# Performance work log

Hardware: AMD Instinct MI355X
Metric: run time of the kernel (lower is better)

## Reference

```python
import jax, jax.numpy as jnp
import numpy as np

INPUT_SIZE = (224, 224)


def setup_inputs() -> dict:
    key = jax.random.key(0)
    k1, k2, k3 = jax.random.split(key, 3)
    feat2 = jax.random.normal(k1, (16, 512, 28, 28), dtype=jnp.float32)
    feat3 = jax.random.normal(k2, (16, 1024, 14, 14), dtype=jnp.float32)
    memory_bank = jax.random.normal(k3, (16384, 1536), dtype=jnp.float32)
    return {"feat2": feat2, "feat3": feat3, "memory_bank": memory_bank}


def reference(feat2, feat3, memory_bank):
    b, c2, h, w = feat2.shape
    c3 = feat3.shape[1]
    # interpolate(feat3, size=(h,w), mode='bilinear', align_corners=False)
    feat3_up = jax.image.resize(feat3, (b, c3, h, w), method='bilinear')
    features = jnp.concatenate([feat2, feat3_up], axis=1)  # [b, c, h, w]
    c = c2 + c3
    feats = features.transpose(0, 2, 3, 1).reshape(-1, c)  # [N, c]
    x_sq = jnp.sum(feats * feats, axis=1, keepdims=True)            # [N, 1]
    m_sq = jnp.sum(memory_bank * memory_bank, axis=1)[None, :]      # [1, M]
    d2 = x_sq + m_sq - 2.0 * (feats @ memory_bank.T)                # [N, M]
    min_d = jnp.sqrt(jnp.maximum(jnp.min(d2, axis=1), 0.0))         # [N]
    anomaly_map = min_d.reshape(b, 1, h, w)
    anomaly_map = jax.image.resize(
        anomaly_map, (b, 1, INPUT_SIZE[0], INPUT_SIZE[1]), method='bilinear')
    pred_score = jnp.max(anomaly_map.reshape(b, -1), axis=1)
    return anomaly_map, pred_score
```

## Files before the change

kernel.cpp:

```cpp
#include <hip/hip_runtime.h>
#include <math.h>

#define N_ROWS 12544
#define C_DIM  1536
#define M_ROWS 16384
#define BATCH  16

#define QS    16.0f
#define S2x2  0.0078125f
#define S2    0.00390625f

typedef int   i32x4 __attribute__((ext_vector_type(4)));
typedef unsigned char u8;
typedef signed char   i8;

__device__ __forceinline__ unsigned fkey(float f) {
  unsigned u = __float_as_uint(f);
  return (u & 0x80000000u) ? ~u : (u | 0x80000000u);
}
__device__ __forceinline__ float funkey(unsigned k) {
  unsigned u = (k & 0x80000000u) ? (k ^ 0x80000000u) : ~k;
  return __uint_as_float(u);
}

__device__ __forceinline__ void gl_lds16(const void* g, void* l) {
  __builtin_amdgcn_global_load_lds(
      (__attribute__((address_space(1))) void*)(g),
      (__attribute__((address_space(3))) void*)(l), 16, 0, 0);
}

__device__ __forceinline__ int quant(float v) {
  int q = __float2int_rn(v * QS);
  return max(-127, min(127, q));
}

#define FSTRIDE 528

__global__ __launch_bounds__(512) void prep_all(
    const float* __restrict__ feat2, const float* __restrict__ feat3,
    const float* __restrict__ mb,
    i8* __restrict__ feats, i8* __restrict__ mbb,
    int* __restrict__ xsqp, float* __restrict__ msq,
    unsigned* __restrict__ dmin, unsigned* __restrict__ score) {
  const int blk = blockIdx.x;
  const int t = threadIdx.x;
  __shared__ u8 fsm[28 * FSTRIDE];
  __shared__ int sxq[28];

  if (blk >= 1344) {
    const int wave = t >> 6, lane = t & 63;
    const int row = (blk - 1344) * 8 + wave;
    const float* in = mb + (size_t)row * C_DIM;
    i8* outp = mbb + (size_t)row * C_DIM;
    float ssq = 0.f;
#pragma unroll
    for (int i = 0; i < 6; i++) {
      const int f4 = lane + 64 * i;
      const float4 v = *(const float4*)(in + f4 * 4);
      int q0 = quant(v.x), q1 = quant(v.y), q2 = quant(v.z), q3 = quant(v.w);
      unsigned w = (unsigned)(q0 & 0xFF) | ((unsigned)(q1 & 0xFF) << 8)
                 | ((unsigned)(q2 & 0xFF) << 16) | ((unsigned)(q3 & 0xFF) << 24);
      *(unsigned*)(outp + f4 * 4) = w;
      ssq += (float)(q0*q0 + q1*q1 + q2*q2 + q3*q3);
    }
    for (int off = 32; off > 0; off >>= 1) ssq += __shfl_down(ssq, off, 64);
    if (lane == 0) msq[row] = S2 * ssq;
  } else {
    const int half = blk % 3, p = blk / 3;
    const int b = p / 28, y = p % 28;
    const int n0 = b * 784 + y * 28;

    const float sy = 0.5f * y - 0.25f;
    const int y0 = (int)floorf(sy); const float fy = sy - (float)y0;
    const int y0c = max(y0, 0), y1c = min(y0 + 1, 13);
    const float wy0 = 1.f - fy, wy1 = fy;

    const int g  = t >> 5;
    const int l2 = t & 31;
    const float sx = 0.5f * l2 - 0.25f;
    const int x0 = (int)floorf(sx); const float fx = sx - (float)x0;
    const int x0c = max(x0, 0), x1c = min(x0 + 1, 13);
    const float wx0 = 1.f - fx, wx1 = fx;

    if (t < 28) sxq[t] = 0;

    if (half == 0) {
      const float* f2b = feat2 + (size_t)b * 512 * 784 + y * 28;
#pragma unroll 4
      for (int i = 0; i < 32; i++) {
        const int c = i * 16 + g;
        if (l2 < 28) {
          float v = f2b[(size_t)c * 784 + l2];
          fsm[l2 * FSTRIDE + c] = (u8)(i8)quant(v);
        }
      }
    } else {
      const int cc0 = (half - 1) * 512;
      const float* f3b = feat3 + (size_t)b * 1024 * 196;
#pragma unroll 4
      for (int i = 0; i < 32; i++) {
        const int cc = cc0 + i * 16 + g;
        const float* f3 = f3b + (size_t)cc * 196;
        float v = 0.f;
        if (l2 < 14)       v = f3[y0c * 14 + l2];
        else if (l2 < 28)  v = f3[y1c * 14 + (l2 - 14)];
        float t0 = wy0 * __shfl(v, x0c, 32)     + wy1 * __shfl(v, 14 + x0c, 32);
        float t1 = wy0 * __shfl(v, x1c, 32)     + wy1 * __shfl(v, 14 + x1c, 32);
        if (l2 < 28) {
          float o = wx0 * t0 + wx1 * t1;
          fsm[l2 * FSTRIDE + (i * 16 + g)] = (u8)(i8)quant(o);
        }
      }
    }
    __syncthreads();

    const int c0 = half * 512;
    i8* orow = feats + (size_t)n0 * C_DIM + c0;
    for (int idx = t; idx < 28 * 32; idx += 512) {
      const int row = idx / 32, col = idx % 32;
      i32x4 wv = *(const i32x4*)(fsm + row * FSTRIDE + col * 16);
      *(i32x4*)(orow + (size_t)row * C_DIM + col * 16) = wv;
      int s = 0;
#pragma unroll
      for (int k = 0; k < 4; k++) {
        const int w = wv[k];
        const int b0 = (int)(i8)(w & 0xFF), b1 = (int)(i8)((w >> 8) & 0xFF);
        const int b2 = (int)(i8)((w >> 16) & 0xFF), b3 = (int)(i8)(w >> 24);
        s += b0*b0 + b1*b1 + b2*b2 + b3*b3;
      }
      atomicAdd(&sxq[row], s);
    }
    __syncthreads();
    if (t < 28) {
      xsqp[half * N_ROWS + n0 + t] = sxq[t];
      if (half == 0) dmin[n0 + t] = 0xFFFFFFFFu;
    }
    if (blk == 0 && t < BATCH) score[t] = 0u;
  }
}

__global__ void gemm_min(const i8* __restrict__ X, const i8* __restrict__ Mb,
                         const float* __restrict__ msq,
                         unsigned* __restrict__ dmin) {
  __shared__ u8 As[16384];
  __shared__ u8 Bs[16384];
  __shared__ unsigned smin[128];
  const int t = threadIdx.x;
  const int bx = blockIdx.x;
  const int mtile = ((bx & 7) << 4) | (bx >> 3);
  const int ntile = blockIdx.y;
  const int lane = t & 63, wave = t >> 6;
  const int wm = wave >> 1, wn = wave & 1;
  if (t < 128) smin[t] = 0xFFFFFFFFu;

  const int row0 = ntile * 128;
  const int col0 = mtile * 128;
  const int s_row = t >> 2;
  const int s_ch  = (t & 3) ^ ((t >> 3) & 3);
  const i8* ga = X  + (size_t)(row0 + s_row) * C_DIM + s_ch * 16;
  const i8* gb = Mb + (size_t)(col0 + s_row) * C_DIM + s_ch * 16;
  u8* la = As + t * 16;
  u8* lb = Bs + t * 16;

  i32x4 acc[4][4];
  const i32x4 zero = {0, 0, 0, 0};
#pragma unroll
  for (int mi = 0; mi < 4; mi++)
#pragma unroll
    for (int ni = 0; ni < 4; ni++) acc[mi][ni] = zero;

  const int quad = lane >> 4, l16 = lane & 15;
  const int fsw = (l16 >> 1) & 3;
  const int slot = ((quad ^ fsw) * 16);
  const u8* arow = As + (wm * 64 + l16) * 64 + slot;
  const u8* brow = Bs + (wn * 64 + l16) * 64 + slot;

  for (int k0 = 0; k0 < C_DIM; k0 += 128) {
    __syncthreads();
    gl_lds16(ga + k0,                    la);
    gl_lds16(ga + 64 * C_DIM + k0,       la + 4096);
    gl_lds16(ga + k0 + 64,               la + 8192);
    gl_lds16(ga + 64 * C_DIM + k0 + 64,  la + 12288);
    gl_lds16(gb + k0,                    lb);
    gl_lds16(gb + 64 * C_DIM + k0,       lb + 4096);
    gl_lds16(gb + k0 + 64,               lb + 8192);
    gl_lds16(gb + 64 * C_DIM + k0 + 64,  lb + 12288);
    __syncthreads();
#pragma unroll
    for (int sub = 0; sub < 2; sub++) {
      i32x4 af[4], bf[4];
#pragma unroll
      for (int mi = 0; mi < 4; mi++)
        af[mi] = *(const i32x4*)(arow + sub * 8192 + mi * 1024);
#pragma unroll
      for (int ni = 0; ni < 4; ni++)
        bf[ni] = *(const i32x4*)(brow + sub * 8192 + ni * 1024);
#pragma unroll
      for (int mi = 0; mi < 4; mi++)
#pragma unroll
        for (int ni = 0; ni < 4; ni++)
          acc[mi][ni] = __builtin_amdgcn_mfma_i32_16x16x64_i8(
              af[mi], bf[ni], acc[mi][ni], 0, 0, 0);
    }
  }

  float msql[4];
#pragma unroll
  for (int ni = 0; ni < 4; ni++)
    msql[ni] = msq[col0 + wn * 64 + ni * 16 + l16];

#pragma unroll
  for (int mi = 0; mi < 4; mi++) {
#pragma unroll
    for (int r = 0; r < 4; r++) {
      float v = msql[0] - S2x2 * (float)acc[mi][0][r];
#pragma unroll
      for (int ni = 1; ni < 4; ni++)
        v = fminf(v, msql[ni] - S2x2 * (float)acc[mi][ni][r]);
      v = fminf(v, __shfl_xor(v, 1, 64));
      v = fminf(v, __shfl_xor(v, 2, 64));
      v = fminf(v, __shfl_xor(v, 4, 64));
      v = fminf(v, __shfl_xor(v, 8, 64));
      if (l16 == 0) {
        int lrow = wm * 64 + mi * 16 + quad * 4 + r;
        atomicMin(&smin[lrow], fkey(v));
      }
    }
  }
  __syncthreads();
  if (t < 128) atomicMin(&dmin[row0 + t], smin[t]);
}

__global__ void finalize(const unsigned* __restrict__ dmin,
                         const int* __restrict__ xsqp,
                         float* __restrict__ out) {
  const int b = blockIdx.x, slice = blockIdx.y, t = threadIdx.x;
  __shared__ float smap[784];
  __shared__ float sred[4];
  for (int i = t; i < 784; i += 256) {
    const int idx = b * 784 + i;
    const int xs = xsqp[idx] + xsqp[N_ROWS + idx] + xsqp[2 * N_ROWS + idx];
    float d2 = S2 * (float)xs + funkey(dmin[idx]);
    smap[i] = sqrtf(fmaxf(d2, 0.f));
  }
  __syncthreads();
  float* omap = out + (size_t)b * 50176;
  float tmax = 0.f;
  const int p0 = slice * 6272;
  for (int p = p0 + t; p < p0 + 6272; p += 256) {
    const int Y = p / 224, Xp = p % 224;
    const float sy = Y * 0.125f - 0.4375f;
    const float sx = Xp * 0.125f - 0.4375f;
    const int y0 = (int)floorf(sy); const float fy = sy - (float)y0;
    const int x0 = (int)floorf(sx); const float fx = sx - (float)x0;
    const int y0c = max(y0, 0), y1c = min(y0 + 1, 27);
    const int x0c = max(x0, 0), x1c = min(x0 + 1, 27);
    float v = (1.f-fy)*((1.f-fx)*smap[y0c*28+x0c] + fx*smap[y0c*28+x1c])
            +      fy *((1.f-fx)*smap[y1c*28+x0c] + fx*smap[y1c*28+x1c]);
    omap[p] = v;
    tmax = fmaxf(tmax, v);
  }
  for (int off = 32; off > 0; off >>= 1)
    tmax = fmaxf(tmax, __shfl_down(tmax, off, 64));
  if ((t & 63) == 0) sred[t >> 6] = tmax;
  __syncthreads();
  if (t == 0) {
    float m = fmaxf(fmaxf(sred[0], sred[1]), fmaxf(sred[2], sred[3]));
    atomicMax((unsigned*)(out + 802816 + b), __float_as_uint(m));
  }
}

extern "C" void kernel_launch(void* const* d_in, const int* in_sizes, int n_in,
                              void* d_out, int out_size, void* d_ws, size_t ws_size,
                              hipStream_t stream) {
  const float* feat2 = (const float*)d_in[0];
  const float* feat3 = (const float*)d_in[1];
  const float* mb    = (const float*)d_in[2];
  char* ws = (char*)d_ws;
  i8*       feats = (i8*)ws;
  i8*       mbb   = (i8*)(ws + 19267584);
  int*      xsqp  = (int*)(ws + 44433408);
  float*    msq   = (float*)(ws + 44583936);
  unsigned* dmin  = (unsigned*)(ws + 44649472);
  float* out = (float*)d_out;

  prep_all<<<1344 + 2048, 512, 0, stream>>>(
      feat2, feat3, mb, feats, mbb, xsqp, msq, dmin,
      (unsigned*)(out + 802816));
  gemm_min<<<dim3(128, 98), 256, 0, stream>>>(feats, mbb, msq, dmin);
  finalize<<<dim3(BATCH, 8), 256, 0, stream>>>(dmin, xsqp, out);
}
```

Measured before the change: 507.4 us.

## Double-buffer GEMM LDS tiles with async prefetch and manual vmcnt waits

Restructures the int8 GEMM main loop into a two-buffer software pipeline over 64-wide K slices. The next slice is loaded global-to-LDS while the current slice runs on MFMA, with explicit s_waitcnt vmcnt and s_barrier in place of paired __syncthreads. The aim is to hide global load latency behind matrix compute. It also adds launch_bounds(256). The risk is correctness of the hand-placed waits and barriers, plus extra barrier count per K step.

```diff
diff --git a/kernel.cpp b/kernel.cpp
--- a/kernel.cpp
+++ b/kernel.cpp
@@ -139,9 +139,9 @@
   }
 }
 
-__global__ void gemm_min(const i8* __restrict__ X, const i8* __restrict__ Mb,
-                         const float* __restrict__ msq,
-                         unsigned* __restrict__ dmin) {
+__global__ __launch_bounds__(256) void gemm_min(
+    const i8* __restrict__ X, const i8* __restrict__ Mb,
+    const float* __restrict__ msq, unsigned* __restrict__ dmin) {
   __shared__ u8 As[16384];
   __shared__ u8 Bs[16384];
   __shared__ unsigned smin[128];
@@ -175,34 +175,52 @@
   const u8* arow = As + (wm * 64 + l16) * 64 + slot;
   const u8* brow = Bs + (wn * 64 + l16) * 64 + slot;
 
-  for (int k0 = 0; k0 < C_DIM; k0 += 128) {
-    __syncthreads();
-    gl_lds16(ga + k0,                    la);
-    gl_lds16(ga + 64 * C_DIM + k0,       la + 4096);
-    gl_lds16(ga + k0 + 64,               la + 8192);
-    gl_lds16(ga + 64 * C_DIM + k0 + 64,  la + 12288);
-    gl_lds16(gb + k0,                    lb);
-    gl_lds16(gb + 64 * C_DIM + k0,       lb + 4096);
-    gl_lds16(gb + k0 + 64,               lb + 8192);
-    gl_lds16(gb + 64 * C_DIM + k0 + 64,  lb + 12288);
-    __syncthreads();
-#pragma unroll
-    for (int sub = 0; sub < 2; sub++) {
-      i32x4 af[4], bf[4];
-#pragma unroll
-      for (int mi = 0; mi < 4; mi++)
-        af[mi] = *(const i32x4*)(arow + sub * 8192 + mi * 1024);
-#pragma unroll
-      for (int ni = 0; ni < 4; ni++)
-        bf[ni] = *(const i32x4*)(brow + sub * 8192 + ni * 1024);
-#pragma unroll
-      for (int mi = 0; mi < 4; mi++)
-#pragma unroll
-        for (int ni = 0; ni < 4; ni++)
-          acc[mi][ni] = __builtin_amdgcn_mfma_i32_16x16x64_i8(
-              af[mi], bf[ni], acc[mi][ni], 0, 0, 0);
-    }
-  }
+#define STAGE(BUF, KS) { \
+    gl_lds16(ga + (KS) * 64,                 la + (BUF) * 8192); \
+    gl_lds16(ga + 64 * C_DIM + (KS) * 64,    la + (BUF) * 8192 + 4096); \
+    gl_lds16(gb + (KS) * 64,                 lb + (BUF) * 8192); \
+    gl_lds16(gb + 64 * C_DIM + (KS) * 64,    lb + (BUF) * 8192 + 4096); }
+#define COMPUTE(BUF) { \
+    i32x4 af[4], bf[4]; \
+    _Pragma("unroll") \
+    for (int mi = 0; mi < 4; mi++) \
+      af[mi] = *(const i32x4*)(arow + (BUF) * 8192 + mi * 1024); \
+    _Pragma("unroll") \
+    for (int ni = 0; ni < 4; ni++) \
+      bf[ni] = *(const i32x4*)(brow + (BUF) * 8192 + ni * 1024); \
+    _Pragma("unroll") \
+    for (int mi = 0; mi < 4; mi++) \
+      _Pragma("unroll") \
+      for (int ni = 0; ni < 4; ni++) \
+        acc[mi][ni] = __builtin_amdgcn_mfma_i32_16x16x64_i8( \
+            af[mi], bf[ni], acc[mi][ni], 0, 0, 0); }
+#define VM4  asm volatile("s_waitcnt vmcnt(4)" ::: "memory")
+#define VM0  asm volatile("s_waitcnt vmcnt(0)" ::: "memory")
+#define BARR asm volatile("s_barrier" ::: "memory")
+
+  STAGE(0, 0);
+  for (int ks = 0; ks < 22; ks += 2) {
+    STAGE(1, ks + 1);
+    VM4; BARR;
+    COMPUTE(0);
+    BARR;
+    STAGE(0, ks + 2);
+    VM4; BARR;
+    COMPUTE(1);
+    BARR;
+  }
+  STAGE(1, 23);
+  VM4; BARR;
+  COMPUTE(0);
+  BARR;
+  VM0; BARR;
+  COMPUTE(1);
+
+#undef BARR
+#undef VM0
+#undef VM4
+#undef COMPUTE
+#undef STAGE
 
   float msql[4];
 #pragma unroll
```

Measured after the change: 564.0 us. 11.1% more time.
